# Optimization experiments

Hardware: AMD Instinct MI355X
Metric: run time of the kernel (lower is better)

## Reference

```python
import jax, jax.numpy as jnp
import numpy as np

D_MODEL = 256
NHEAD = 8
HEAD_DIM = D_MODEL // NHEAD
EPS = 1e-6
LN_EPS = 1e-5


def embed_rotary(x, cos, sin):
    # x, cos, sin: [N, L, C]; rotate even/odd pairs (Lepard-style RoFPE)
    x2 = jnp.stack([-x[..., 1::2], x[..., ::2]], axis=-1).reshape(x.shape)
    return x * cos + x2 * sin


def layer_norm(x, g, b):
    m = jnp.mean(x, axis=-1, keepdims=True)
    v = jnp.mean((x - m) ** 2, axis=-1, keepdims=True)
    return (x - m) / jnp.sqrt(v + LN_EPS) * g + b


def setup_inputs() -> dict:
    key = jax.random.key(0)
    ks = jax.random.split(key, 12)
    N, L, S, C = 8, 4096, 4096, D_MODEL
    s = 1.0 / np.sqrt(C)
    return {
        "x": jax.random.normal(ks[0], (N, L, C), jnp.float32),
        "source": jax.random.normal(ks[1], (N, S, C), jnp.float32),
        "x_pe": jax.random.normal(ks[2], (N, L, C, 2), jnp.float32),
        "source_pe": jax.random.normal(ks[3], (N, S, C, 2), jnp.float32),
        "Wq": jax.random.normal(ks[4], (C, C), jnp.float32) * s,
        "Wk": jax.random.normal(ks[5], (C, C), jnp.float32) * s,
        "Wv": jax.random.normal(ks[6], (C, C), jnp.float32) * s,
        "Wm": jax.random.normal(ks[7], (C, C), jnp.float32) * s,
        "W1": jax.random.normal(ks[8], (2 * C, 2 * C), jnp.float32) * s,
        "W2": jax.random.normal(ks[9], (2 * C, C), jnp.float32) * s,
        "ln1_g": jnp.ones((C,), jnp.float32),
        "ln1_b": jnp.zeros((C,), jnp.float32),
        "ln2_g": jnp.ones((C,), jnp.float32),
        "ln2_b": jnp.zeros((C,), jnp.float32),
    }


def reference(x, source, x_pe, source_pe, Wq, Wk, Wv, Wm, W1, W2, ln1_g, ln1_b, ln2_g, ln2_b):
    N, L, C = x.shape
    S = source.shape[1]
    H, D = NHEAD, HEAD_DIM

    query = x @ Wq           # [N, L, C]
    key = source @ Wk        # [N, S, C]
    value = source @ Wv      # [N, S, C]

    # ELU+1 feature maps (on pre-rotary projections)
    Q = jax.nn.elu(query) + 1.0
    K = jax.nn.elu(key) + 1.0

    q_cos, q_sin = x_pe[..., 0], x_pe[..., 1]
    k_cos, k_sin = source_pe[..., 0], source_pe[..., 1]
    Q_pos = embed_rotary(query, q_cos, q_sin)
    K_pos = embed_rotary(key, k_cos, k_sin)
    value = embed_rotary(value, k_cos, k_sin)

    Q = Q.reshape(N, L, H, D)
    K = K.reshape(N, S, H, D)
    Q_pos = Q_pos.reshape(N, L, H, D)
    K_pos = K_pos.reshape(N, S, H, D)
    value = value.reshape(N, S, H, D)

    values = value / S
    KV = jnp.einsum('nshd,nshv->nhdv', K_pos, values)          # [N, H, D, D]
    Z = 1.0 / (jnp.einsum('nlhd,nhd->nlh', Q, K.sum(axis=1)) + EPS)
    queried = jnp.einsum('nlhd,nhdv->nlhv', Q_pos, KV) * Z[..., None] * S  # [N, L, H, D]

    message = queried.reshape(N, L, C) @ Wm
    message = layer_norm(message, ln1_g, ln1_b)
    h = jnp.concatenate([x, message], axis=2) @ W1             # [N, L, 2C]
    h = jax.nn.relu(h)
    message = h @ W2                                            # [N, L, C]
    message = layer_norm(message, ln2_g, ln2_b)
    return x + message
```

## Files before the change

### kernel.cpp

```cpp
#include <hip/hip_runtime.h>

typedef __attribute__((ext_vector_type(8))) short bf16x8;
typedef __attribute__((ext_vector_type(4))) float f32x4;

__device__ __forceinline__ float bf2f(unsigned short b) {
    unsigned u = ((unsigned)b) << 16; float f;
    __builtin_memcpy(&f, &u, 4); return f;
}
__device__ __forceinline__ unsigned short f2bf(float f) {
    unsigned u; __builtin_memcpy(&u, &f, 4);
    unsigned r = u + 0x7FFFu + ((u >> 16) & 1u);
    return (unsigned short)(r >> 16);
}

__device__ __forceinline__ void async_copy16(const unsigned short* g, unsigned short* l) {
    __builtin_amdgcn_global_load_lds(
        (const __attribute__((address_space(1))) unsigned int*)g,
        (__attribute__((address_space(3))) unsigned int*)l, 16, 0, 0);
}

#define EPI_F32 0
#define EPI_RELU_BF16 1
#define EPI_ROTARY_Q 2
#define EPI_ROTARY_KV 3

template <int EPI>
__global__ __launch_bounds__(256) void gemm_bt(
    const unsigned short* __restrict__ A, int lda,
    const unsigned short* __restrict__ B, int K, int N,
    float* __restrict__ Cf, unsigned short* __restrict__ Cb,
    const float* __restrict__ pe,
    const float* __restrict__ Ksum, float* __restrict__ Zbuf,
    unsigned short* __restrict__ out_pos,
    unsigned short* __restrict__ outT_k,
    unsigned short* __restrict__ outT_v,
    unsigned short* __restrict__ out_elu)
{
    __shared__ unsigned short Asm[128 * 32];
    __shared__ unsigned short Bsm[128 * 32];
    const int t = threadIdx.x;
    const int lane = t & 63, w = t >> 6;
    const int wm = w & 1, wn = w >> 1;
    const int quad = lane >> 4, low = lane & 15;
    const int m0 = blockIdx.x * 128, n0 = blockIdx.y * 128;

    f32x4 acc[4][4];
#pragma unroll
    for (int i = 0; i < 4; i++)
#pragma unroll
        for (int j = 0; j < 4; j++) acc[i][j] = (f32x4){0.f, 0.f, 0.f, 0.f};

    for (int k0 = 0; k0 < K; k0 += 32) {
        __syncthreads();
#pragma unroll
        for (int i = 0; i < 2; i++) {
            const int chunk = i * 256 + t;
            const int row = chunk >> 2, part = chunk & 3;
            async_copy16(A + (size_t)(m0 + row) * lda + k0 + part * 8,
                         Asm + (i * 256 + w * 64) * 8);
            async_copy16(B + (size_t)(n0 + row) * K + k0 + part * 8,
                         Bsm + (i * 256 + w * 64) * 8);
        }
        __syncthreads();
        bf16x8 a[4], b[4];
#pragma unroll
        for (int mi = 0; mi < 4; mi++)
            a[mi] = *(const bf16x8*)&Asm[(wm * 64 + mi * 16 + low) * 32 + quad * 8];
#pragma unroll
        for (int ni = 0; ni < 4; ni++)
            b[ni] = *(const bf16x8*)&Bsm[(wn * 64 + ni * 16 + low) * 32 + quad * 8];
#pragma unroll
        for (int mi = 0; mi < 4; mi++)
#pragma unroll
            for (int ni = 0; ni < 4; ni++)
                acc[mi][ni] = __builtin_amdgcn_mfma_f32_16x16x32_bf16(a[mi], b[ni], acc[mi][ni], 0, 0, 0);
    }

    const int gmb = m0 + wm * 64, gnb = n0 + wn * 64;

    if constexpr (EPI == EPI_F32) {
#pragma unroll
        for (int mi = 0; mi < 4; mi++)
#pragma unroll
            for (int ni = 0; ni < 4; ni++)
#pragma unroll
                for (int r = 0; r < 4; r++) {
                    const int row = gmb + mi * 16 + quad * 4 + r;
                    const int col = gnb + ni * 16 + low;
                    Cf[(size_t)row * N + col] = acc[mi][ni][r];
                }
    } else if constexpr (EPI == EPI_RELU_BF16) {
#pragma unroll
        for (int mi = 0; mi < 4; mi++)
#pragma unroll
            for (int ni = 0; ni < 4; ni++)
#pragma unroll
                for (int r = 0; r < 4; r++) {
                    const int row = gmb + mi * 16 + quad * 4 + r;
                    const int col = gnb + ni * 16 + low;
                    const float v = acc[mi][ni][r];
                    Cb[(size_t)row * N + col] = f2bf(v > 0.f ? v : 0.f);
                }
    } else if constexpr (EPI == EPI_ROTARY_Q) {
#pragma unroll
        for (int mi = 0; mi < 4; mi++) {
#pragma unroll
            for (int j = 0; j < 2; j++) {
                float zp[4] = {0.f, 0.f, 0.f, 0.f};
#pragma unroll
                for (int nn = 0; nn < 2; nn++) {
                    const int ni = j * 2 + nn;
                    const int c = gnb + ni * 16 + low;
#pragma unroll
                    for (int r = 0; r < 4; r++) {
                        const int row = gmb + mi * 16 + quad * 4 + r;
                        const float v = acc[mi][ni][r];
                        const float pp = __shfl_xor(v, 1);
                        const float2 cs = *(const float2*)&pe[((size_t)row * 256 + c) * 2];
                        const float x2 = (c & 1) ? pp : -pp;
                        out_pos[(size_t)row * 256 + c] = f2bf(v * cs.x + x2 * cs.y);
                        const float e = (v > 0.f ? v + 1.f : __expf(v)) * Ksum[(row >> 12) * 256 + c];
                        zp[r] += e;
                    }
                }
#pragma unroll
                for (int r = 0; r < 4; r++) {
                    float s = zp[r];
                    s += __shfl_xor(s, 1); s += __shfl_xor(s, 2);
                    s += __shfl_xor(s, 4); s += __shfl_xor(s, 8);
                    if (low == 0) {
                        const int row = gmb + mi * 16 + quad * 4 + r;
                        Zbuf[(size_t)row * 8 + ((gnb + j * 32) >> 5)] = 1.f / (s + 1e-6f);
                    }
                }
            }
        }
    } else {
#pragma unroll
        for (int mi = 0; mi < 4; mi++) {
            const int row0 = gmb + mi * 16 + quad * 4;
            const int n = row0 >> 12, s = row0 & 4095;
#pragma unroll
            for (int ni = 0; ni < 4; ni++) {
                const int colg = gnb + ni * 16 + low;
                const int c = colg & 255;
                unsigned short rpack[4];
#pragma unroll
                for (int r = 0; r < 4; r++) {
                    const int row = row0 + r;
                    const float v = acc[mi][ni][r];
                    const float pp = __shfl_xor(v, 1);
                    const float2 cs = *(const float2*)&pe[((size_t)row * 256 + c) * 2];
                    const float x2 = (c & 1) ? pp : -pp;
                    rpack[r] = f2bf(v * cs.x + x2 * cs.y);
                    if (colg < 256)
                        out_elu[(size_t)row * 256 + c] = f2bf(v > 0.f ? v + 1.f : __expf(v));
                }
                unsigned short* dT = (colg < 256) ? outT_k : outT_v;
                *(uint2*)&dT[((size_t)(n * 256 + c)) * 4096 + s] = *(const uint2*)rpack;
            }
        }
    }
}

__global__ void transp_bf16(const float* __restrict__ W, unsigned short* __restrict__ WT, int K, int N) {
    const int idx = blockIdx.x * 256 + threadIdx.x;
    if (idx >= K * N) return;
    const int n = idx / K, k = idx - n * K;
    WT[idx] = f2bf(W[(size_t)k * N + n]);
}

__global__ void conv_bf16(const float* __restrict__ src, unsigned short* __restrict__ dst, int dstride) {
    const int idx = blockIdx.x * 256 + threadIdx.x;
    const int row = idx >> 6;
    const int c0 = (idx & 63) * 4;
    const float4 v = *(const float4*)&src[(size_t)row * 256 + c0];
    unsigned short o[4] = {f2bf(v.x), f2bf(v.y), f2bf(v.z), f2bf(v.w)};
    *(uint2*)&dst[(size_t)row * dstride + c0] = *(const uint2*)o;
}

__global__ void ksum_kernel(const unsigned short* __restrict__ Kelu, float* __restrict__ Ksum) {
    const int n = blockIdx.x, chunk = blockIdx.y, c = threadIdx.x;
    float s = 0.f;
    const size_t base = ((size_t)(n * 4096 + chunk * 128)) * 256 + c;
    for (int i = 0; i < 128; i++) s += bf2f(Kelu[base + (size_t)i * 256]);
    atomicAdd(&Ksum[n * 256 + c], s);
}

__global__ __launch_bounds__(256) void kv2_kernel(const unsigned short* __restrict__ KposT,
                                                  const unsigned short* __restrict__ VrotT,
                                                  float* __restrict__ KVT) {
    const int nh = blockIdx.x, sc = blockIdx.y;
    const int t = threadIdx.x, lane = t & 63, w = t >> 6;
    const int quad = lane >> 4, low = lane & 15;
    const unsigned short* Abase = KposT + (size_t)nh * 32 * 4096;
    const unsigned short* Bbase = VrotT + (size_t)nh * 32 * 4096;
    const int sbase = sc * 1024 + w * 256;

    f32x4 acc[2][2];
#pragma unroll
    for (int i = 0; i < 2; i++)
#pragma unroll
        for (int j = 0; j < 2; j++) acc[i][j] = (f32x4){0.f, 0.f, 0.f, 0.f};

    for (int s0 = 0; s0 < 256; s0 += 32) {
        const int sk = sbase + s0 + quad * 8;
        bf16x8 a[2], b[2];
#pragma unroll
        for (int mi = 0; mi < 2; mi++)
            a[mi] = *(const bf16x8*)&Abase[(size_t)(mi * 16 + low) * 4096 + sk];
#pragma unroll
        for (int ni = 0; ni < 2; ni++)
            b[ni] = *(const bf16x8*)&Bbase[(size_t)(ni * 16 + low) * 4096 + sk];
#pragma unroll
        for (int mi = 0; mi < 2; mi++)
#pragma unroll
            for (int ni = 0; ni < 2; ni++)
                acc[mi][ni] = __builtin_amdgcn_mfma_f32_16x16x32_bf16(a[mi], b[ni], acc[mi][ni], 0, 0, 0);
    }

    __shared__ float red[4][1024];
#pragma unroll
    for (int mi = 0; mi < 2; mi++)
#pragma unroll
        for (int ni = 0; ni < 2; ni++)
#pragma unroll
            for (int r = 0; r < 4; r++)
                red[w][(mi * 16 + quad * 4 + r) * 32 + ni * 16 + low] = acc[mi][ni][r];
    __syncthreads();
#pragma unroll
    for (int k = 0; k < 4; k++) {
        const int i = t + k * 256;
        const float s = red[0][i] + red[1][i] + red[2][i] + red[3][i];
        atomicAdd(&KVT[(size_t)nh * 1024 + (size_t)(i & 31) * 32 + (i >> 5)], s);
    }
}

__global__ __launch_bounds__(256) void attn_out_kernel(const unsigned short* __restrict__ Qpos,
                                                       const float* __restrict__ KVT,
                                                       const float* __restrict__ Zbuf,
                                                       unsigned short* __restrict__ Qrd) {
    const int h = blockIdx.y, mt = blockIdx.x;
    const int t = threadIdx.x, lane = t & 63, w = t >> 6;
    const int quad = lane >> 4, low = lane & 15;
    const int rbase = mt * 256 + w * 64;
    const int n = rbase >> 12;

    bf16x8 b[2];
#pragma unroll
    for (int ni = 0; ni < 2; ni++) {
        const float* src = &KVT[((size_t)(n * 8 + h) * 32 + ni * 16 + low) * 32 + quad * 8];
        short tmp[8];
#pragma unroll
        for (int j = 0; j < 8; j++) tmp[j] = (short)f2bf(src[j]);
        __builtin_memcpy(&b[ni], tmp, 16);
    }

    f32x4 acc[4][2];
#pragma unroll
    for (int i = 0; i < 4; i++)
#pragma unroll
        for (int j = 0; j < 2; j++) acc[i][j] = (f32x4){0.f, 0.f, 0.f, 0.f};

#pragma unroll
    for (int mi = 0; mi < 4; mi++) {
        const bf16x8 a = *(const bf16x8*)&Qpos[((size_t)(rbase + mi * 16 + low)) * 256 + h * 32 + quad * 8];
#pragma unroll
        for (int ni = 0; ni < 2; ni++)
            acc[mi][ni] = __builtin_amdgcn_mfma_f32_16x16x32_bf16(a, b[ni], acc[mi][ni], 0, 0, 0);
    }

#pragma unroll
    for (int mi = 0; mi < 4; mi++)
#pragma unroll
        for (int ni = 0; ni < 2; ni++)
#pragma unroll
            for (int r = 0; r < 4; r++) {
                const int row = rbase + mi * 16 + quad * 4 + r;
                const int col = h * 32 + ni * 16 + low;
                Qrd[(size_t)row * 256 + col] = f2bf(acc[mi][ni][r] * Zbuf[(size_t)row * 8 + h]);
            }
}

__global__ void ln1_kernel(const float* __restrict__ msg, unsigned short* __restrict__ a2,
                           const float* __restrict__ g, const float* __restrict__ b) {
    const int row = blockIdx.x, t = threadIdx.x;
    const float v = msg[(size_t)row * 256 + t];
    float s1 = v, s2 = v * v;
#pragma unroll
    for (int off = 32; off >= 1; off >>= 1) { s1 += __shfl_xor(s1, off); s2 += __shfl_xor(s2, off); }
    __shared__ float red[8];
    const int w = t >> 6;
    if ((t & 63) == 0) { red[w * 2] = s1; red[w * 2 + 1] = s2; }
    __syncthreads();
    s1 = red[0] + red[2] + red[4] + red[6];
    s2 = red[1] + red[3] + red[5] + red[7];
    const float mean = s1 * (1.f / 256.f);
    const float var = s2 * (1.f / 256.f) - mean * mean;
    const float rstd = rsqrtf(var + 1e-5f);
    a2[(size_t)row * 512 + 256 + t] = f2bf((v - mean) * rstd * g[t] + b[t]);
}

__global__ void ln2_res_kernel(const float* __restrict__ msg, const float* __restrict__ x,
                               const float* __restrict__ g, const float* __restrict__ b,
                               float* __restrict__ out) {
    const int row = blockIdx.x, t = threadIdx.x;
    const float v = msg[(size_t)row * 256 + t];
    float s1 = v, s2 = v * v;
#pragma unroll
    for (int off = 32; off >= 1; off >>= 1) { s1 += __shfl_xor(s1, off); s2 += __shfl_xor(s2, off); }
    __shared__ float red[8];
    const int w = t >> 6;
    if ((t & 63) == 0) { red[w * 2] = s1; red[w * 2 + 1] = s2; }
    __syncthreads();
    s1 = red[0] + red[2] + red[4] + red[6];
    s2 = red[1] + red[3] + red[5] + red[7];
    const float mean = s1 * (1.f / 256.f);
    const float var = s2 * (1.f / 256.f) - mean * mean;
    const float rstd = rsqrtf(var + 1e-5f);
    out[(size_t)row * 256 + t] = x[(size_t)row * 256 + t] + (v - mean) * rstd * g[t] + b[t];
}

extern "C" void kernel_launch(void* const* d_in, const int* in_sizes, int n_in,
                              void* d_out, int out_size, void* d_ws, size_t ws_size,
                              hipStream_t stream) {
    const float* x   = (const float*)d_in[0];
    const float* src = (const float*)d_in[1];
    const float* xpe = (const float*)d_in[2];
    const float* spe = (const float*)d_in[3];
    const float* Wq  = (const float*)d_in[4];
    const float* Wk  = (const float*)d_in[5];
    const float* Wv  = (const float*)d_in[6];
    const float* Wm  = (const float*)d_in[7];
    const float* W1  = (const float*)d_in[8];
    const float* W2  = (const float*)d_in[9];
    const float* g1  = (const float*)d_in[10];
    const float* b1  = (const float*)d_in[11];
    const float* g2  = (const float*)d_in[12];
    const float* b2  = (const float*)d_in[13];

    char* p = (char*)d_ws;
    unsigned short* WqT  = (unsigned short*)p; p += 256 * 256 * 2;
    unsigned short* WkvT = (unsigned short*)p; p += 512 * 256 * 2;
    unsigned short* WmT  = (unsigned short*)p; p += 256 * 256 * 2;
    unsigned short* W1T  = (unsigned short*)p; p += 512 * 512 * 2;
    unsigned short* W2T  = (unsigned short*)p; p += 256 * 512 * 2;
    float* KVT  = (float*)p; p += 64 * 1024 * 4;
    float* Ksum = (float*)p; p += 8 * 256 * 4;
    float* Zbuf = (float*)p; p += (size_t)32768 * 8 * 4;
    unsigned short* A2   = (unsigned short*)p; p += (size_t)32768 * 512 * 2;
    unsigned short* srcB = (unsigned short*)p; p += (size_t)32768 * 256 * 2;
    unsigned short* Kelu  = (unsigned short*)p; p += (size_t)32768 * 256 * 2;
    unsigned short* KposT = (unsigned short*)p; p += (size_t)32768 * 256 * 2;
    unsigned short* VrotT = (unsigned short*)p; p += (size_t)32768 * 256 * 2;
    unsigned short* Qpos  = (unsigned short*)p; p += (size_t)32768 * 256 * 2;
    unsigned short* Qrd   = (unsigned short*)p; p += (size_t)32768 * 256 * 2;
    float* msg1 = (float*)Kelu;
    unsigned short* hbuf = (unsigned short*)VrotT;
    float* msg2 = msg1;

    hipMemsetAsync(KVT, 0, 64 * 1024 * 4 + 8 * 256 * 4, stream);

    transp_bf16<<<256, 256, 0, stream>>>(Wq, WqT, 256, 256);
    transp_bf16<<<256, 256, 0, stream>>>(Wk, WkvT, 256, 256);
    transp_bf16<<<256, 256, 0, stream>>>(Wv, WkvT + 256 * 256, 256, 256);
    transp_bf16<<<256, 256, 0, stream>>>(Wm, WmT, 256, 256);
    transp_bf16<<<1024, 256, 0, stream>>>(W1, W1T, 512, 512);
    transp_bf16<<<512, 256, 0, stream>>>(W2, W2T, 512, 256);
    conv_bf16<<<8192, 256, 0, stream>>>(x, A2, 512);
    conv_bf16<<<8192, 256, 0, stream>>>(src, srcB, 256);

    gemm_bt<EPI_ROTARY_KV><<<dim3(256, 4), 256, 0, stream>>>(srcB, 256, WkvT, 256, 512,
        nullptr, nullptr, spe, nullptr, nullptr, nullptr, KposT, VrotT, Kelu);
    ksum_kernel<<<dim3(8, 32), 256, 0, stream>>>(Kelu, Ksum);
    gemm_bt<EPI_ROTARY_Q><<<dim3(256, 2), 256, 0, stream>>>(A2, 512, WqT, 256, 256,
        nullptr, nullptr, xpe, Ksum, Zbuf, Qpos, nullptr, nullptr, nullptr);

    kv2_kernel<<<dim3(64, 4), 256, 0, stream>>>(KposT, VrotT, KVT);
    attn_out_kernel<<<dim3(128, 8), 256, 0, stream>>>(Qpos, KVT, Zbuf, Qrd);

    gemm_bt<EPI_F32><<<dim3(256, 2), 256, 0, stream>>>(Qrd, 256, WmT, 256, 256,
        msg1, nullptr, nullptr, nullptr, nullptr, nullptr, nullptr, nullptr, nullptr);
    ln1_kernel<<<32768, 256, 0, stream>>>(msg1, A2, g1, b1);
    gemm_bt<EPI_RELU_BF16><<<dim3(256, 4), 256, 0, stream>>>(A2, 512, W1T, 512, 512,
        nullptr, hbuf, nullptr, nullptr, nullptr, nullptr, nullptr, nullptr, nullptr);
    gemm_bt<EPI_F32><<<dim3(256, 2), 256, 0, stream>>>(hbuf, 512, W2T, 512, 256,
        msg2, nullptr, nullptr, nullptr, nullptr, nullptr, nullptr, nullptr, nullptr);
    ln2_res_kernel<<<32768, 256, 0, stream>>>(msg2, x, g2, b2, (float*)d_out);
}
```

Baseline: 457.8 us.

## Fuse layernorms and K-sum into GEMM epilogues with permuted channel layout

Weight columns are permuted so each lane holds even/odd rotary pairs, letting epilogues apply the rotary embedding without shuffles and write packed bf16 pairs. LayerNorm 1 and LayerNorm 2 plus the residual are fused into 64x256 GEMM tiles, so the fp32 message intermediates and the separate LN kernels go away. The ELU key sum is accumulated with atomics in the KV epilogue, which drops the Kelu buffer and the ksum kernel. K and V are stored in a blocked layout for kv2, and the weight transposes plus the memset are merged into one prep kernel. The trade-off is that 64x256 tiles launch fewer blocks and the atomics make the sum order nondeterministic.

```diff
diff --git a/kernel.cpp b/kernel.cpp
--- a/kernel.cpp
+++ b/kernel.cpp
@@ -12,6 +12,10 @@
     unsigned r = u + 0x7FFFu + ((u >> 16) & 1u);
     return (unsigned short)(r >> 16);
 }
+__device__ __forceinline__ unsigned packbf(float a, float b) {
+    return (unsigned)f2bf(a) | ((unsigned)f2bf(b) << 16);
+}
+__device__ __forceinline__ float elu1(float v) { return v > 0.f ? v + 1.f : __expf(v); }
 
 __device__ __forceinline__ void async_copy16(const unsigned short* g, unsigned short* l) {
     __builtin_amdgcn_global_load_lds(
@@ -19,155 +23,231 @@
         (__attribute__((address_space(3))) unsigned int*)l, 16, 0, 0);
 }
 
-#define EPI_F32 0
-#define EPI_RELU_BF16 1
-#define EPI_ROTARY_Q 2
-#define EPI_ROTARY_KV 3
-
-template <int EPI>
+__device__ __host__ __forceinline__ int chan_of(int tc) {
+    return (tc & ~63) | ((tc & 15) << 1) | ((tc >> 4) & 1) | (((tc >> 5) & 1) << 5);
+}
+__device__ __forceinline__ int chan_even(int gnb, int p, int low) {
+    const int tc = gnb + 32 * p + low;
+    return (tc & ~63) | ((tc & 15) << 1) | (((tc >> 5) & 1) << 5);
+}
+
+#define EPI_RELU 0
+#define EPI_Q 1
+#define EPI_KV 2
+#define EPI_LN1 3
+#define EPI_LN2RES 4
+
+template <int MT, int NT, int EPI>
 __global__ __launch_bounds__(256) void gemm_bt(
     const unsigned short* __restrict__ A, int lda,
-    const unsigned short* __restrict__ B, int K, int N,
-    float* __restrict__ Cf, unsigned short* __restrict__ Cb,
+    const unsigned short* __restrict__ B, int K,
+    unsigned short* __restrict__ Cb, int ldc,
     const float* __restrict__ pe,
-    const float* __restrict__ Ksum, float* __restrict__ Zbuf,
-    unsigned short* __restrict__ out_pos,
-    unsigned short* __restrict__ outT_k,
-    unsigned short* __restrict__ outT_v,
-    unsigned short* __restrict__ out_elu)
+    const float* __restrict__ KsumC, float* __restrict__ KsumA,
+    float* __restrict__ Zbuf, unsigned short* __restrict__ Qpos,
+    unsigned short* __restrict__ KF, unsigned short* __restrict__ VF,
+    const float* __restrict__ g, const float* __restrict__ bta,
+    unsigned short* __restrict__ A2out,
+    const float* __restrict__ xres, float* __restrict__ outF)
 {
-    __shared__ unsigned short Asm[128 * 32];
-    __shared__ unsigned short Bsm[128 * 32];
+    constexpr int WM = MT / 2, WN = NT / 2, MI = WM / 16, NI = WN / 16;
+    __shared__ unsigned short Asm[MT * 32];
+    __shared__ unsigned short Bsm[NT * 32];
     const int t = threadIdx.x;
     const int lane = t & 63, w = t >> 6;
     const int wm = w & 1, wn = w >> 1;
     const int quad = lane >> 4, low = lane & 15;
-    const int m0 = blockIdx.x * 128, n0 = blockIdx.y * 128;
-
-    f32x4 acc[4][4];
-#pragma unroll
-    for (int i = 0; i < 4; i++)
-#pragma unroll
-        for (int j = 0; j < 4; j++) acc[i][j] = (f32x4){0.f, 0.f, 0.f, 0.f};
+    const int m0 = blockIdx.x * MT, n0 = blockIdx.y * NT;
+
+    f32x4 acc[MI][NI];
+#pragma unroll
+    for (int i = 0; i < MI; i++)
+#pragma unroll
+        for (int j = 0; j < NI; j++) acc[i][j] = (f32x4){0.f, 0.f, 0.f, 0.f};
 
     for (int k0 = 0; k0 < K; k0 += 32) {
         __syncthreads();
 #pragma unroll
-        for (int i = 0; i < 2; i++) {
+        for (int i = 0; i < MT / 64; i++) {
             const int chunk = i * 256 + t;
             const int row = chunk >> 2, part = chunk & 3;
             async_copy16(A + (size_t)(m0 + row) * lda + k0 + part * 8,
                          Asm + (i * 256 + w * 64) * 8);
+        }
+#pragma unroll
+        for (int i = 0; i < NT / 64; i++) {
+            const int chunk = i * 256 + t;
+            const int row = chunk >> 2, part = chunk & 3;
             async_copy16(B + (size_t)(n0 + row) * K + k0 + part * 8,
                          Bsm + (i * 256 + w * 64) * 8);
         }
         __syncthreads();
-        bf16x8 a[4], b[4];
-#pragma unroll
-        for (int mi = 0; mi < 4; mi++)
-            a[mi] = *(const bf16x8*)&Asm[(wm * 64 + mi * 16 + low) * 32 + quad * 8];
-#pragma unroll
-        for (int ni = 0; ni < 4; ni++)
-            b[ni] = *(const bf16x8*)&Bsm[(wn * 64 + ni * 16 + low) * 32 + quad * 8];
-#pragma unroll
-        for (int mi = 0; mi < 4; mi++)
-#pragma unroll
-            for (int ni = 0; ni < 4; ni++)
+        bf16x8 a[MI], b[NI];
+#pragma unroll
+        for (int mi = 0; mi < MI; mi++)
+            a[mi] = *(const bf16x8*)&Asm[(wm * WM + mi * 16 + low) * 32 + quad * 8];
+#pragma unroll
+        for (int ni = 0; ni < NI; ni++)
+            b[ni] = *(const bf16x8*)&Bsm[(wn * WN + ni * 16 + low) * 32 + quad * 8];
+#pragma unroll
+        for (int mi = 0; mi < MI; mi++)
+#pragma unroll
+            for (int ni = 0; ni < NI; ni++)
                 acc[mi][ni] = __builtin_amdgcn_mfma_f32_16x16x32_bf16(a[mi], b[ni], acc[mi][ni], 0, 0, 0);
     }
 
-    const int gmb = m0 + wm * 64, gnb = n0 + wn * 64;
-
-    if constexpr (EPI == EPI_F32) {
-#pragma unroll
-        for (int mi = 0; mi < 4; mi++)
-#pragma unroll
-            for (int ni = 0; ni < 4; ni++)
+    const int gmb = m0 + wm * WM, gnb = n0 + wn * WN;
+
+    if constexpr (EPI == EPI_RELU) {
+#pragma unroll
+        for (int mi = 0; mi < MI; mi++)
+#pragma unroll
+            for (int p = 0; p < NI / 2; p++) {
+                const int c_e = chan_even(gnb, p, low);
 #pragma unroll
                 for (int r = 0; r < 4; r++) {
                     const int row = gmb + mi * 16 + quad * 4 + r;
-                    const int col = gnb + ni * 16 + low;
-                    Cf[(size_t)row * N + col] = acc[mi][ni][r];
-                }
-    } else if constexpr (EPI == EPI_RELU_BF16) {
-#pragma unroll
-        for (int mi = 0; mi < 4; mi++)
-#pragma unroll
-            for (int ni = 0; ni < 4; ni++)
+                    const float ve = acc[mi][2 * p][r], vo = acc[mi][2 * p + 1][r];
+                    *(unsigned*)&Cb[(size_t)row * ldc + c_e] =
+                        packbf(ve > 0.f ? ve : 0.f, vo > 0.f ? vo : 0.f);
+                }
+            }
+    } else if constexpr (EPI == EPI_Q) {
+        const int n = m0 >> 12;
+#pragma unroll
+        for (int p = 0; p < NI / 2; p++) {
+            const int c_e = chan_even(gnb, p, low);
+            const int head = c_e >> 5;
+            const float2 ks = *(const float2*)&KsumC[n * 256 + c_e];
+#pragma unroll
+            for (int mi = 0; mi < MI; mi++) {
 #pragma unroll
                 for (int r = 0; r < 4; r++) {
                     const int row = gmb + mi * 16 + quad * 4 + r;
-                    const int col = gnb + ni * 16 + low;
-                    const float v = acc[mi][ni][r];
-                    Cb[(size_t)row * N + col] = f2bf(v > 0.f ? v : 0.f);
-                }
-    } else if constexpr (EPI == EPI_ROTARY_Q) {
-#pragma unroll
-        for (int mi = 0; mi < 4; mi++) {
-#pragma unroll
-            for (int j = 0; j < 2; j++) {
-                float zp[4] = {0.f, 0.f, 0.f, 0.f};
-#pragma unroll
-                for (int nn = 0; nn < 2; nn++) {
-                    const int ni = j * 2 + nn;
-                    const int c = gnb + ni * 16 + low;
-#pragma unroll
-                    for (int r = 0; r < 4; r++) {
-                        const int row = gmb + mi * 16 + quad * 4 + r;
-                        const float v = acc[mi][ni][r];
-                        const float pp = __shfl_xor(v, 1);
-                        const float2 cs = *(const float2*)&pe[((size_t)row * 256 + c) * 2];
-                        const float x2 = (c & 1) ? pp : -pp;
-                        out_pos[(size_t)row * 256 + c] = f2bf(v * cs.x + x2 * cs.y);
-                        const float e = (v > 0.f ? v + 1.f : __expf(v)) * Ksum[(row >> 12) * 256 + c];
-                        zp[r] += e;
-                    }
-                }
+                    const float4 cs = *(const float4*)&pe[((size_t)row * 256 + c_e) * 2];
+                    const float ve = acc[mi][2 * p][r], vo = acc[mi][2 * p + 1][r];
+                    *(unsigned*)&Qpos[(size_t)row * 256 + c_e] =
+                        packbf(ve * cs.x - vo * cs.y, vo * cs.z + ve * cs.w);
+                    float z = elu1(ve) * ks.x + elu1(vo) * ks.y;
+                    z += __shfl_xor(z, 1); z += __shfl_xor(z, 2);
+                    z += __shfl_xor(z, 4); z += __shfl_xor(z, 8);
+                    if (low == 0) Zbuf[(size_t)row * 8 + head] = 1.f / (z + 1e-6f);
+                }
+            }
+        }
+    } else if constexpr (EPI == EPI_KV) {
+        const int n = m0 >> 12;
+#pragma unroll
+        for (int p = 0; p < NI / 2; p++) {
+            const int c_full = chan_even(gnb, p, low);
+            const bool isK = c_full < 256;
+            const int c = c_full & 255;
+            const int nh = n * 8 + (c >> 5), d = c & 31;
+            unsigned short* dst = isK ? KF : VF;
+            float kel_e = 0.f, kel_o = 0.f;
+#pragma unroll
+            for (int mi = 0; mi < MI; mi++) {
+                const int row0 = gmb + mi * 16 + quad * 4;
+                const int s0 = row0 & 4095;
+                unsigned short pk[8];
 #pragma unroll
                 for (int r = 0; r < 4; r++) {
-                    float s = zp[r];
-                    s += __shfl_xor(s, 1); s += __shfl_xor(s, 2);
-                    s += __shfl_xor(s, 4); s += __shfl_xor(s, 8);
-                    if (low == 0) {
-                        const int row = gmb + mi * 16 + quad * 4 + r;
-                        Zbuf[(size_t)row * 8 + ((gnb + j * 32) >> 5)] = 1.f / (s + 1e-6f);
-                    }
+                    const int row = row0 + r;
+                    const float4 cs = *(const float4*)&pe[((size_t)row * 256 + c) * 2];
+                    const float ve = acc[mi][2 * p][r], vo = acc[mi][2 * p + 1][r];
+                    pk[r]     = f2bf(ve * cs.x - vo * cs.y);
+                    pk[4 + r] = f2bf(vo * cs.z + ve * cs.w);
+                    if (isK) { kel_e += elu1(ve); kel_o += elu1(vo); }
+                }
+                const size_t base = ((size_t)nh * 512 + (s0 >> 3)) * 32;
+                *(uint2*)&dst[(base + d) * 8 + (s0 & 7)]     = *(const uint2*)&pk[0];
+                *(uint2*)&dst[(base + d + 1) * 8 + (s0 & 7)] = *(const uint2*)&pk[4];
+            }
+            if (isK) {
+                kel_e += __shfl_xor(kel_e, 16); kel_e += __shfl_xor(kel_e, 32);
+                kel_o += __shfl_xor(kel_o, 16); kel_o += __shfl_xor(kel_o, 32);
+                if (quad == 0) {
+                    atomicAdd(&KsumA[n * 256 + c], kel_e);
+                    atomicAdd(&KsumA[n * 256 + c + 1], kel_o);
                 }
             }
         }
     } else {
-#pragma unroll
-        for (int mi = 0; mi < 4; mi++) {
-            const int row0 = gmb + mi * 16 + quad * 4;
-            const int n = row0 >> 12, s = row0 & 4095;
-#pragma unroll
-            for (int ni = 0; ni < 4; ni++) {
-                const int colg = gnb + ni * 16 + low;
-                const int c = colg & 255;
-                unsigned short rpack[4];
-#pragma unroll
-                for (int r = 0; r < 4; r++) {
-                    const int row = row0 + r;
+        __shared__ float2 lnp[2][64];
+        __syncthreads();
+#pragma unroll
+        for (int mi = 0; mi < MI; mi++)
+#pragma unroll
+            for (int r = 0; r < 4; r++) {
+                float s1 = 0.f, s2 = 0.f;
+#pragma unroll
+                for (int ni = 0; ni < NI; ni++) {
                     const float v = acc[mi][ni][r];
-                    const float pp = __shfl_xor(v, 1);
-                    const float2 cs = *(const float2*)&pe[((size_t)row * 256 + c) * 2];
-                    const float x2 = (c & 1) ? pp : -pp;
-                    rpack[r] = f2bf(v * cs.x + x2 * cs.y);
-                    if (colg < 256)
-                        out_elu[(size_t)row * 256 + c] = f2bf(v > 0.f ? v + 1.f : __expf(v));
-                }
-                unsigned short* dT = (colg < 256) ? outT_k : outT_v;
-                *(uint2*)&dT[((size_t)(n * 256 + c)) * 4096 + s] = *(const uint2*)rpack;
-            }
-        }
-    }
-}
-
-__global__ void transp_bf16(const float* __restrict__ W, unsigned short* __restrict__ WT, int K, int N) {
+                    s1 += v; s2 += v * v;
+                }
+                s1 += __shfl_xor(s1, 1); s2 += __shfl_xor(s2, 1);
+                s1 += __shfl_xor(s1, 2); s2 += __shfl_xor(s2, 2);
+                s1 += __shfl_xor(s1, 4); s2 += __shfl_xor(s2, 4);
+                s1 += __shfl_xor(s1, 8); s2 += __shfl_xor(s2, 8);
+                if (low == 0) lnp[wn][wm * WM + mi * 16 + quad * 4 + r] = make_float2(s1, s2);
+            }
+        __syncthreads();
+#pragma unroll
+        for (int mi = 0; mi < MI; mi++)
+#pragma unroll
+            for (int r = 0; r < 4; r++) {
+                const int rl = wm * WM + mi * 16 + quad * 4 + r;
+                const int row = m0 + rl;
+                const float2 pa = lnp[0][rl], pb = lnp[1][rl];
+                const float mean = (pa.x + pb.x) * (1.f / 256.f);
+                const float var = (pa.y + pb.y) * (1.f / 256.f) - mean * mean;
+                const float rstd = rsqrtf(var + 1e-5f);
+#pragma unroll
+                for (int p = 0; p < NI / 2; p++) {
+                    const int c_e = chan_even(gnb, p, low);
+                    const float2 gg = *(const float2*)&g[c_e];
+                    const float2 bb = *(const float2*)&bta[c_e];
+                    const float ve = acc[mi][2 * p][r], vo = acc[mi][2 * p + 1][r];
+                    const float oe = (ve - mean) * rstd * gg.x + bb.x;
+                    const float oo = (vo - mean) * rstd * gg.y + bb.y;
+                    if constexpr (EPI == EPI_LN1) {
+                        *(unsigned*)&A2out[(size_t)row * 512 + 256 + c_e] = packbf(oe, oo);
+                    } else {
+                        const float2 xv = *(const float2*)&xres[(size_t)row * 256 + c_e];
+                        float2 o; o.x = xv.x + oe; o.y = xv.y + oo;
+                        *(float2*)&outF[(size_t)row * 256 + c_e] = o;
+                    }
+                }
+            }
+    }
+}
+
+__global__ void prep_weights(const float* __restrict__ Wq, const float* __restrict__ Wk,
+                             const float* __restrict__ Wv, const float* __restrict__ Wm,
+                             const float* __restrict__ W1, const float* __restrict__ W2,
+                             unsigned short* __restrict__ WqT, unsigned short* __restrict__ WkvT,
+                             unsigned short* __restrict__ WmT, unsigned short* __restrict__ W1T,
+                             unsigned short* __restrict__ W2T, float* __restrict__ zero_base) {
     const int idx = blockIdx.x * 256 + threadIdx.x;
-    if (idx >= K * N) return;
-    const int n = idx / K, k = idx - n * K;
-    WT[idx] = f2bf(W[(size_t)k * N + n]);
+    if (idx < 65536) {
+        const int tc = idx >> 8, k = idx & 255;
+        WqT[idx] = f2bf(Wq[(size_t)k * 256 + chan_of(tc)]);
+    } else if (idx < 196608) {
+        const int i = idx - 65536, tc = i >> 8, k = i & 255;
+        const int c = chan_of(tc);
+        WkvT[i] = f2bf(c < 256 ? Wk[(size_t)k * 256 + c] : Wv[(size_t)k * 256 + (c - 256)]);
+    } else if (idx < 262144) {
+        const int i = idx - 196608, tc = i >> 8, k = i & 255;
+        WmT[i] = f2bf(Wm[(size_t)k * 256 + chan_of(tc)]);
+    } else if (idx < 524288) {
+        const int i = idx - 262144, tc = i >> 9, k = i & 511;
+        W1T[i] = f2bf(W1[(size_t)k * 512 + chan_of(tc)]);
+    } else if (idx < 655360) {
+        const int i = idx - 524288, tc = i >> 9, k = i & 511;
+        W2T[i] = f2bf(W2[(size_t)k * 256 + chan_of(tc)]);
+    } else {
+        zero_base[idx - 655360] = 0.f;
+    }
 }
 
 __global__ void conv_bf16(const float* __restrict__ src, unsigned short* __restrict__ dst, int dstride) {
@@ -179,22 +259,12 @@
     *(uint2*)&dst[(size_t)row * dstride + c0] = *(const uint2*)o;
 }
 
-__global__ void ksum_kernel(const unsigned short* __restrict__ Kelu, float* __restrict__ Ksum) {
-    const int n = blockIdx.x, chunk = blockIdx.y, c = threadIdx.x;
-    float s = 0.f;
-    const size_t base = ((size_t)(n * 4096 + chunk * 128)) * 256 + c;
-    for (int i = 0; i < 128; i++) s += bf2f(Kelu[base + (size_t)i * 256]);
-    atomicAdd(&Ksum[n * 256 + c], s);
-}
-
-__global__ __launch_bounds__(256) void kv2_kernel(const unsigned short* __restrict__ KposT,
-                                                  const unsigned short* __restrict__ VrotT,
+__global__ __launch_bounds__(256) void kv2_kernel(const unsigned short* __restrict__ KF,
+                                                  const unsigned short* __restrict__ VF,
                                                   float* __restrict__ KVT) {
     const int nh = blockIdx.x, sc = blockIdx.y;
     const int t = threadIdx.x, lane = t & 63, w = t >> 6;
     const int quad = lane >> 4, low = lane & 15;
-    const unsigned short* Abase = KposT + (size_t)nh * 32 * 4096;
-    const unsigned short* Bbase = VrotT + (size_t)nh * 32 * 4096;
     const int sbase = sc * 1024 + w * 256;
 
     f32x4 acc[2][2];
@@ -205,13 +275,14 @@
 
     for (int s0 = 0; s0 < 256; s0 += 32) {
         const int sk = sbase + s0 + quad * 8;
+        const size_t cb = ((size_t)nh * 512 + (sk >> 3)) * 32;
         bf16x8 a[2], b[2];
 #pragma unroll
         for (int mi = 0; mi < 2; mi++)
-            a[mi] = *(const bf16x8*)&Abase[(size_t)(mi * 16 + low) * 4096 + sk];
+            a[mi] = *(const bf16x8*)&KF[(cb + mi * 16 + low) * 8];
 #pragma unroll
         for (int ni = 0; ni < 2; ni++)
-            b[ni] = *(const bf16x8*)&Bbase[(size_t)(ni * 16 + low) * 4096 + sk];
+            b[ni] = *(const bf16x8*)&VF[(cb + ni * 16 + low) * 8];
 #pragma unroll
         for (int mi = 0; mi < 2; mi++)
 #pragma unroll
@@ -280,45 +351,6 @@
                 const int col = h * 32 + ni * 16 + low;
                 Qrd[(size_t)row * 256 + col] = f2bf(acc[mi][ni][r] * Zbuf[(size_t)row * 8 + h]);
             }
-}
-
-__global__ void ln1_kernel(const float* __restrict__ msg, unsigned short* __restrict__ a2,
-                           const float* __restrict__ g, const float* __restrict__ b) {
-    const int row = blockIdx.x, t = threadIdx.x;
-    const float v = msg[(size_t)row * 256 + t];
-    float s1 = v, s2 = v * v;
-#pragma unroll
-    for (int off = 32; off >= 1; off >>= 1) { s1 += __shfl_xor(s1, off); s2 += __shfl_xor(s2, off); }
-    __shared__ float red[8];
-    const int w = t >> 6;
-    if ((t & 63) == 0) { red[w * 2] = s1; red[w * 2 + 1] = s2; }
-    __syncthreads();
-    s1 = red[0] + red[2] + red[4] + red[6];
-    s2 = red[1] + red[3] + red[5] + red[7];
-    const float mean = s1 * (1.f / 256.f);
-    const float var = s2 * (1.f / 256.f) - mean * mean;
-    const float rstd = rsqrtf(var + 1e-5f);
-    a2[(size_t)row * 512 + 256 + t] = f2bf((v - mean) * rstd * g[t] + b[t]);
-}
-
-__global__ void ln2_res_kernel(const float* __restrict__ msg, const float* __restrict__ x,
-                               const float* __restrict__ g, const float* __restrict__ b,
-                               float* __restrict__ out) {
-    const int row = blockIdx.x, t = threadIdx.x;
-    const float v = msg[(size_t)row * 256 + t];
-    float s1 = v, s2 = v * v;
-#pragma unroll
-    for (int off = 32; off >= 1; off >>= 1) { s1 += __shfl_xor(s1, off); s2 += __shfl_xor(s2, off); }
-    __shared__ float red[8];
-    const int w = t >> 6;
-    if ((t & 63) == 0) { red[w * 2] = s1; red[w * 2 + 1] = s2; }
-    __syncthreads();
-    s1 = red[0] + red[2] + red[4] + red[6];
-    s2 = red[1] + red[3] + red[5] + red[7];
-    const float mean = s1 * (1.f / 256.f);
-    const float var = s2 * (1.f / 256.f) - mean * mean;
-    const float rstd = rsqrtf(var + 1e-5f);
-    out[(size_t)row * 256 + t] = x[(size_t)row * 256 + t] + (v - mean) * rstd * g[t] + b[t];
 }
 
 extern "C" void kernel_launch(void* const* d_in, const int* in_sizes, int n_in,
@@ -350,41 +382,37 @@
     float* Zbuf = (float*)p; p += (size_t)32768 * 8 * 4;
     unsigned short* A2   = (unsigned short*)p; p += (size_t)32768 * 512 * 2;
     unsigned short* srcB = (unsigned short*)p; p += (size_t)32768 * 256 * 2;
-    unsigned short* Kelu  = (unsigned short*)p; p += (size_t)32768 * 256 * 2;
-    unsigned short* KposT = (unsigned short*)p; p += (size_t)32768 * 256 * 2;
-    unsigned short* VrotT = (unsigned short*)p; p += (size_t)32768 * 256 * 2;
-    unsigned short* Qpos  = (unsigned short*)p; p += (size_t)32768 * 256 * 2;
-    unsigned short* Qrd   = (unsigned short*)p; p += (size_t)32768 * 256 * 2;
-    float* msg1 = (float*)Kelu;
-    unsigned short* hbuf = (unsigned short*)VrotT;
-    float* msg2 = msg1;
-
-    hipMemsetAsync(KVT, 0, 64 * 1024 * 4 + 8 * 256 * 4, stream);
-
-    transp_bf16<<<256, 256, 0, stream>>>(Wq, WqT, 256, 256);
-    transp_bf16<<<256, 256, 0, stream>>>(Wk, WkvT, 256, 256);
-    transp_bf16<<<256, 256, 0, stream>>>(Wv, WkvT + 256 * 256, 256, 256);
-    transp_bf16<<<256, 256, 0, stream>>>(Wm, WmT, 256, 256);
-    transp_bf16<<<1024, 256, 0, stream>>>(W1, W1T, 512, 512);
-    transp_bf16<<<512, 256, 0, stream>>>(W2, W2T, 512, 256);
+    unsigned short* KF   = (unsigned short*)p; p += (size_t)32768 * 256 * 2;
+    unsigned short* VF   = (unsigned short*)p; p += (size_t)32768 * 256 * 2;
+    unsigned short* Qpos = (unsigned short*)p; p += (size_t)32768 * 256 * 2;
+    unsigned short* Qrd  = (unsigned short*)p; p += (size_t)32768 * 256 * 2;
+    unsigned short* hbuf = KF;
+
+    prep_weights<<<2824, 256, 0, stream>>>(Wq, Wk, Wv, Wm, W1, W2,
+                                           WqT, WkvT, WmT, W1T, W2T, KVT);
     conv_bf16<<<8192, 256, 0, stream>>>(x, A2, 512);
     conv_bf16<<<8192, 256, 0, stream>>>(src, srcB, 256);
 
-    gemm_bt<EPI_ROTARY_KV><<<dim3(256, 4), 256, 0, stream>>>(srcB, 256, WkvT, 256, 512,
-        nullptr, nullptr, spe, nullptr, nullptr, nullptr, KposT, VrotT, Kelu);
-    ksum_kernel<<<dim3(8, 32), 256, 0, stream>>>(Kelu, Ksum);
-    gemm_bt<EPI_ROTARY_Q><<<dim3(256, 2), 256, 0, stream>>>(A2, 512, WqT, 256, 256,
-        nullptr, nullptr, xpe, Ksum, Zbuf, Qpos, nullptr, nullptr, nullptr);
-
-    kv2_kernel<<<dim3(64, 4), 256, 0, stream>>>(KposT, VrotT, KVT);
+    gemm_bt<128, 128, EPI_KV><<<dim3(256, 4), 256, 0, stream>>>(
+        srcB, 256, WkvT, 256, nullptr, 0, spe, nullptr, Ksum,
+        nullptr, nullptr, KF, VF, nullptr, nullptr, nullptr, nullptr, nullptr);
+    kv2_kernel<<<dim3(64, 4), 256, 0, stream>>>(KF, VF, KVT);
+
+    gemm_bt<128, 128, EPI_Q><<<dim3(256, 2), 256, 0, stream>>>(
+        A2, 512, WqT, 256, nullptr, 0, xpe, Ksum, nullptr,
+        Zbuf, Qpos, nullptr, nullptr, nullptr, nullptr, nullptr, nullptr, nullptr);
+
     attn_out_kernel<<<dim3(128, 8), 256, 0, stream>>>(Qpos, KVT, Zbuf, Qrd);
 
-    gemm_bt<EPI_F32><<<dim3(256, 2), 256, 0, stream>>>(Qrd, 256, WmT, 256, 256,
-        msg1, nullptr, nullptr, nullptr, nullptr, nullptr, nullptr, nullptr, nullptr);
-    ln1_kernel<<<32768, 256, 0, stream>>>(msg1, A2, g1, b1);
-    gemm_bt<EPI_RELU_BF16><<<dim3(256, 4), 256, 0, stream>>>(A2, 512, W1T, 512, 512,
-        nullptr, hbuf, nullptr, nullptr, nullptr, nullptr, nullptr, nullptr, nullptr);
-    gemm_bt<EPI_F32><<<dim3(256, 2), 256, 0, stream>>>(hbuf, 512, W2T, 512, 256,
-        msg2, nullptr, nullptr, nullptr, nullptr, nullptr, nullptr, nullptr, nullptr);
-    ln2_res_kernel<<<32768, 256, 0, stream>>>(msg2, x, g2, b2, (float*)d_out);
-}
+    gemm_bt<64, 256, EPI_LN1><<<512, 256, 0, stream>>>(
+        Qrd, 256, WmT, 256, nullptr, 0, nullptr, nullptr, nullptr,
+        nullptr, nullptr, nullptr, nullptr, g1, b1, A2, nullptr, nullptr);
+
+    gemm_bt<128, 128, EPI_RELU><<<dim3(256, 4), 256, 0, stream>>>(
+        A2, 512, W1T, 512, hbuf, 512, nullptr, nullptr, nullptr,
+        nullptr, nullptr, nullptr, nullptr, nullptr, nullptr, nullptr, nullptr, nullptr);
+
+    gemm_bt<64, 256, EPI_LN2RES><<<512, 256, 0, stream>>>(
+        hbuf, 512, W2T, 512, nullptr, 0, nullptr, nullptr, nullptr,
+        nullptr, nullptr, nullptr, nullptr, g2, b2, nullptr, x, (float*)d_out);
+}
```

New measurement: 406.7 us. 1.13x faster.
